# Performance work log

Measured on AMD Instinct MI355X. Metric: run time of the kernel, lower is better.

## Reference

```python
import jax, jax.numpy as jnp
import numpy as np

WIN = 20  # patch_project window_size
HID = 128


def _lstm_layer(x, w_ih, w_hh, b_ih, b_hh):
    """x: [B,T,D] -> (outputs [B,T,H], final h [B,H]). PyTorch gate order i,f,g,o."""
    B = x.shape[0]
    H = w_hh.shape[1]
    # precompute input contribution for all timesteps: [B,T,4H]
    x_pre = jnp.einsum('btd,gd->btg', x, w_ih) + b_ih + b_hh

    def step(carry, xp):
        h, c = carry
        gates = xp + h @ w_hh.T  # [B,4H]
        i, f, g, o = jnp.split(gates, 4, axis=-1)
        i = jax.nn.sigmoid(i)
        f = jax.nn.sigmoid(f)
        g = jnp.tanh(g)
        o = jax.nn.sigmoid(o)
        c = f * c + i * g
        h = o * jnp.tanh(c)
        return (h, c), h

    h0 = jnp.zeros((B, H), x.dtype)
    c0 = jnp.zeros((B, H), x.dtype)
    (h_f, _), ys = jax.lax.scan(step, (h0, c0), x_pre.transpose(1, 0, 2))
    return ys.transpose(1, 0, 2), h_f


def setup_inputs() -> dict:
    key = jax.random.key(0)
    ks = jax.random.split(key, 20)
    B, S, C = 64, 2048, 32
    D_in = WIN * C          # 640
    D_p = D_in // 2         # 320
    H = HID
    label_len = 48
    s = 0.02
    inp = {
        'inputs': jax.random.normal(ks[0], (B, S, C), jnp.float32),
        '_x': jnp.zeros((B, 4), jnp.float32),
        'y': jnp.zeros((B, label_len), jnp.float32),
        '_y': jnp.zeros((B, 4), jnp.float32),
        'proj_w': jax.random.normal(ks[1], (D_p, D_in), jnp.float32) * s,
        'proj_b': jax.random.normal(ks[2], (D_p,), jnp.float32) * s,
        'w_ih0': jax.random.normal(ks[3], (4 * H, D_p), jnp.float32) * s,
        'w_hh0': jax.random.normal(ks[4], (4 * H, H), jnp.float32) * s,
        'b_ih0': jax.random.normal(ks[5], (4 * H,), jnp.float32) * s,
        'b_hh0': jax.random.normal(ks[6], (4 * H,), jnp.float32) * s,
        'w_ih_rest': jax.random.normal(ks[7], (3, 4 * H, H), jnp.float32) * s,
        'w_hh_rest': jax.random.normal(ks[8], (3, 4 * H, H), jnp.float32) * s,
        'b_ih_rest': jax.random.normal(ks[9], (3, 4 * H), jnp.float32) * s,
        'b_hh_rest': jax.random.normal(ks[10], (3, 4 * H), jnp.float32) * s,
        'out_w': jax.random.normal(ks[11], (label_len, H), jnp.float32) * s,
        'out_b': jax.random.normal(ks[12], (label_len,), jnp.float32) * s,
    }
    return inp


def reference(inputs, _x, y, _y, proj_w, proj_b, w_ih0, w_hh0, b_ih0, b_hh0,
              w_ih_rest, w_hh_rest, b_ih_rest, b_hh_rest, out_w, out_b):
    B, S, C = inputs.shape
    L_out = S - WIN
    idx = jnp.arange(L_out)[:, None] + jnp.arange(WIN)[None, :]
    windows = inputs[:, idx, :].reshape(B, L_out, WIN * C)
    # projection1 (dropout is inference no-op)
    x = jnp.einsum('btd,pd->btp', windows, proj_w) + proj_b
    # 4-layer LSTM (dropout between layers is inference no-op)
    x, h = _lstm_layer(x, w_ih0, w_hh0, b_ih0, b_hh0)
    for l in range(3):
        x, h = _lstm_layer(x, w_ih_rest[l], w_hh_rest[l], b_ih_rest[l], b_hh_rest[l])
    # final hidden state of last layer -> [B,1,H] -> output layer -> [B,1,label_len]
    out = h[:, None, :] @ out_w.T + out_b
    return out
```

## Files before the change

### kernel.cpp

```cpp
#include <hip/hip_runtime.h>
#include <stdint.h>
#include <stddef.h>

typedef __bf16 bf16_t;
typedef bf16_t bf16x8 __attribute__((ext_vector_type(8)));
typedef bf16_t bf16x4 __attribute__((ext_vector_type(4)));
typedef float  f32x4  __attribute__((ext_vector_type(4)));

#define T_STEPS 2028
#define SEQ     2048
#define CIN     32
#define NG      32
#define MB      2
#define CH      32
#define NCH     64
#define RING    4

#define OFF_EFFW   0u
#define OFF_BIAS   655360u
#define OFF_WHH    663552u
#define OFF_WIH    1187840u
#define OFF_HFIN   1581056u
#define OFF_CNT    1613824u
#define OFF_XRING  1638400u
#define OFF_YRING  35192832u

__device__ __forceinline__ int endk(int k) {
  int e = (k + 1) * CH;
  return e > T_STEPS ? T_STEPS : e;
}

__device__ __forceinline__ void spin_ge(uint32_t* p, uint32_t tgt) {
  while (atomicAdd(p, 0u) < tgt) __builtin_amdgcn_s_sleep(2);
}
__device__ __forceinline__ void publish(uint32_t* p, uint32_t v) {
  __builtin_amdgcn_fence(__ATOMIC_RELEASE, "agent");
  atomicMax(p, v);
}

__device__ __forceinline__ float fsigm(float x) {
  return __builtin_amdgcn_rcpf(1.0f + __builtin_amdgcn_exp2f(x * -1.44269504089f));
}
__device__ __forceinline__ float ftanh(float x) {
  return 1.0f - 2.0f * __builtin_amdgcn_rcpf(1.0f + __builtin_amdgcn_exp2f(x * 2.88539008178f));
}

__device__ __forceinline__ bf16x8 ldg8(const bf16_t* p) { return *(const bf16x8*)p; }
__device__ __forceinline__ bf16x4 ldg4(const bf16_t* p) { return *(const bf16x4*)p; }

__device__ __forceinline__ bf16x8 ldg_cvt8(const float* p) {
  const f32x4 a = *(const f32x4*)p;
  const f32x4 b = *(const f32x4*)(p + 4);
  bf16x8 r;
  r[0] = (bf16_t)a[0]; r[1] = (bf16_t)a[1]; r[2] = (bf16_t)a[2]; r[3] = (bf16_t)a[3];
  r[4] = (bf16_t)b[0]; r[5] = (bf16_t)b[1]; r[6] = (bf16_t)b[2]; r[7] = (bf16_t)b[3];
  return r;
}


__global__ void k_prep_misc(const float* __restrict__ w_hh0,
                            const float* __restrict__ w_ih_rest,
                            const float* __restrict__ w_hh_rest,
                            const float* __restrict__ b_ih_rest,
                            const float* __restrict__ b_hh_rest,
                            uint8_t* __restrict__ ws) {
  const int bid = blockIdx.x;
  const int l = bid >> 9;
  const int p = bid & 511;
  const int orig = (p & 3) * 128 + (p >> 2);
  const int tid = threadIdx.x;
  bf16_t* whh = (bf16_t*)(ws + OFF_WHH);
  bf16_t* wih = (bf16_t*)(ws + OFF_WIH);
  float* bias = (float*)(ws + OFF_BIAS);
  const float* src = (l == 0) ? (w_hh0 + orig * 128)
                              : (w_hh_rest + ((size_t)(l - 1) * 512 + orig) * 128);
  whh[((size_t)l * 512 + p) * 128 + tid] = (bf16_t)src[tid];
  if (l < 3)
    wih[((size_t)l * 512 + p) * 128 + tid] = (bf16_t)w_ih_rest[((size_t)l * 512 + orig) * 128 + tid];
  if (l >= 1 && tid == 0)
    bias[l * 512 + p] = b_ih_rest[(l - 1) * 512 + orig] + b_hh_rest[(l - 1) * 512 + orig];
  if (bid == 0) {
    uint32_t* cnt = (uint32_t*)(ws + OFF_CNT);
    for (int i = tid; i < 12 * 32 * 16; i += 128) cnt[i] = 0;
  }
}

__global__ void k_prep_effw(const float* __restrict__ proj_w,
                            const float* __restrict__ proj_b,
                            const float* __restrict__ w_ih0,
                            const float* __restrict__ b_ih0,
                            const float* __restrict__ b_hh0,
                            uint8_t* __restrict__ ws) {
  __shared__ float wr[320];
  const int p = blockIdx.x;
  const int orig = (p & 3) * 128 + (p >> 2);
  const int tid = threadIdx.x;
  for (int i = tid; i < 320; i += 256) wr[i] = w_ih0[(size_t)orig * 320 + i];
  __syncthreads();
  bf16_t* effw = (bf16_t*)(ws + OFF_EFFW);
  for (int kk = tid; kk < 640; kk += 256) {
    float a = 0.f;
    for (int z = 0; z < 320; ++z) a += wr[z] * proj_w[(size_t)z * 640 + kk];
    effw[(size_t)p * 640 + kk] = (bf16_t)a;
  }
  if (tid == 0) {
    float a = 0.f;
    for (int z = 0; z < 320; ++z) a += wr[z] * proj_b[z];
    ((float*)(ws + OFF_BIAS))[p] = a + b_ih0[orig] + b_hh0[orig];
  }
}

__global__ __launch_bounds__(256, 1) void k_pipeline(const float* __restrict__ in,
                                                     uint8_t* __restrict__ ws) {
  __shared__ __align__(16) bf16_t h_lds[2][16][136];
  __shared__ f32x4 gate_buf[4][2][32];

  const int s = blockIdx.x >> 5;
  const int g = blockIdx.x & 31;
  const int tid = threadIdx.x;
  const int lane = tid & 63;
  const int w = tid >> 6;
  const int q = lane >> 4;
  const int ln = lane & 15;

  uint32_t* cnt = (uint32_t*)(ws + OFF_CNT);
  bf16_t* xring = (bf16_t*)(ws + OFF_XRING);
  bf16_t* yring = (bf16_t*)(ws + OFF_YRING);

  if (s == 0) {
    const bf16_t* effw = (const bf16_t*)(ws + OFF_EFFW);
    uint32_t* my = cnt + (0 * NG + g) * 16;
    uint32_t* guard = cnt + (1 * NG + g) * 16;
    for (int k = 0; k < NCH; ++k) {
      if (tid == 0 && k >= RING) spin_ge(guard, (uint32_t)endk(k - RING));
      __syncthreads();
      const int t0 = k * CH;
      f32x4 acc[4][8];
#pragma unroll
      for (int mt = 0; mt < 4; ++mt)
#pragma unroll
        for (int nt = 0; nt < 8; ++nt) acc[mt][nt] = (f32x4){0.f, 0.f, 0.f, 0.f};
#pragma unroll
      for (int kt = 0; kt < 20; ++kt) {
        bf16x8 bfr[8];
#pragma unroll
        for (int nt = 0; nt < 8; ++nt)
          bfr[nt] = ldg8(effw + (size_t)((w * 8 + nt) * 16 + ln) * 640 + kt * 32 + q * 8);
#pragma unroll
        for (int mt = 0; mt < 4; ++mt) {
          int m = mt * 16 + ln;
          int trel = m >> 1, bb = m & 1;
          int tt = t0 + trel; if (tt > T_STEPS - 1) tt = T_STEPS - 1;
          bf16x8 afr = ldg_cvt8(in + (size_t)((g * MB + bb) * SEQ + tt + kt) * CIN + q * 8);
#pragma unroll
          for (int nt = 0; nt < 8; ++nt)
            acc[mt][nt] = __builtin_amdgcn_mfma_f32_16x16x32_bf16(afr, bfr[nt], acc[mt][nt], 0, 0, 0);
        }
      }
      bf16_t* xs = xring + (size_t)((0 * NG + g) * RING + (k & 3)) * (64 * 512);
#pragma unroll
      for (int mt = 0; mt < 4; ++mt)
#pragma unroll
        for (int nt = 0; nt < 8; ++nt)
#pragma unroll
          for (int r = 0; r < 4; ++r)
            xs[(size_t)(mt * 16 + q * 4 + r) * 512 + (w * 8 + nt) * 16 + ln] = (bf16_t)acc[mt][nt][r];
      __syncthreads();
      if (tid == 0) publish(my, (uint32_t)endk(k));
    }
  } else if (s <= 4) {
    const int l = s - 1;
    const bf16_t* whh = (const bf16_t*)(ws + OFF_WHH) + (size_t)l * 512 * 128;
    bf16x8 wfr[8][4];
#pragma unroll
    for (int mt = 0; mt < 8; ++mt)
#pragma unroll
      for (int kt = 0; kt < 4; ++kt)
        wfr[mt][kt] = ldg8(whh + (size_t)(w * 128 + mt * 16 + ln) * 128 + kt * 32 + q * 8);
    const int b_ep = lane >> 5;
    const int j_loc = lane & 31;
    const int jg = w * 32 + j_loc;
    f32x4 biasq = *(const f32x4*)((const float*)(ws + OFF_BIAS) + l * 512 + 4 * jg);
    float c = 0.f;
    {
      bf16_t* hz = &h_lds[0][0][0];
      for (int i = tid; i < 2 * 16 * 136; i += 256) hz[i] = (bf16_t)0.f;
    }
    __syncthreads();
    uint32_t* my = cnt + ((1 + l) * NG + g) * 16;
    uint32_t* prod = (l == 0) ? (cnt + (0 * NG + g) * 16) : (cnt + ((4 + l) * NG + g) * 16);
    uint32_t* yguard = cnt + ((5 + l) * NG + g) * 16;
    float* hfin = (float*)(ws + OFF_HFIN);
    const int ly = (l < 3) ? l : 0;

    for (int k = 0; k < NCH; ++k) {
      const int t0 = k * CH;
      const int tlen = (T_STEPS - t0 < CH) ? (T_STEPS - t0) : CH;
      if (tid == 0) {
        spin_ge(prod, (uint32_t)(t0 + tlen));
        if (l < 3 && k >= RING) spin_ge(yguard, (uint32_t)endk(k - RING));
        __builtin_amdgcn_fence(__ATOMIC_ACQUIRE, "agent");
      }
      __syncthreads();
      const bf16_t* xlane = xring + (size_t)((l * NG + g) * RING + (k & 3)) * (64 * 512)
                            + b_ep * 512 + 4 * jg;
      bf16_t* ylane = yring + (size_t)((ly * NG + g) * RING + (k & 3)) * (64 * 128)
                      + b_ep * 128 + jg;

      if (tlen == CH) {
        for (int half = 0; half < 2; ++half) {
          const int tb = t0 + half * 16;
          bf16x4 xq[16];
#pragma unroll
          for (int t = 0; t < 16; ++t) xq[t] = ldg4(xlane + (size_t)(half * 16 + t) * 1024);
          bf16_t yv[16];
#pragma unroll
          for (int t = 0; t < 16; ++t) {
            const int buf = (tb + t) & 1;
            f32x4 acc[8];
#pragma unroll
            for (int mt = 0; mt < 8; ++mt) acc[mt] = (f32x4){0.f, 0.f, 0.f, 0.f};
#pragma unroll
            for (int kt = 0; kt < 3; ++kt) {
              bf16x8 hk = *(const bf16x8*)&h_lds[buf][ln][kt * 32 + q * 8];
#pragma unroll
              for (int mt = 0; mt < 8; ++mt)
                acc[mt] = __builtin_amdgcn_mfma_f32_16x16x32_bf16(wfr[mt][kt], hk, acc[mt], 0, 0, 0);
            }
            {
              bf16x8 hk3 = *(const bf16x8*)&h_lds[buf][ln][3 * 32 + q * 8];
#pragma unroll
              for (int mt = 0; mt < 8; ++mt) {
                acc[mt] = __builtin_amdgcn_mfma_f32_16x16x32_bf16(wfr[mt][3], hk3, acc[mt], 0, 0, 0);
                if (ln < MB) gate_buf[w][ln][mt * 4 + q] = acc[mt];
              }
            }
            f32x4 gq = gate_buf[w][b_ep][j_loc];
            float gi = fsigm(gq[0] + (float)xq[t][0] + biasq[0]);
            float gf = fsigm(gq[1] + (float)xq[t][1] + biasq[1]);
            float gg = ftanh(gq[2] + (float)xq[t][2] + biasq[2]);
            float go = fsigm(gq[3] + (float)xq[t][3] + biasq[3]);
            c = gf * c + gi * gg;
            float hv = go * ftanh(c);
            h_lds[buf ^ 1][b_ep][jg] = (bf16_t)hv;
            yv[t] = (bf16_t)hv;
            asm volatile("s_waitcnt lgkmcnt(0)\n\ts_barrier" ::: "memory");
          }
          if (l < 3) {
#pragma unroll
            for (int t = 0; t < 16; ++t)
              ylane[(size_t)(half * 16 + t) * 256] = yv[t];
          }
        }
      } else {
        for (int trel = 0; trel < tlen; ++trel) {
          const int t = t0 + trel;
          const int buf = t & 1;
          bf16x4 xqs = ldg4(xlane + (size_t)trel * 1024);
          f32x4 acc[8];
#pragma unroll
          for (int mt = 0; mt < 8; ++mt) acc[mt] = (f32x4){0.f, 0.f, 0.f, 0.f};
#pragma unroll
          for (int kt = 0; kt < 4; ++kt) {
            bf16x8 hk = *(const bf16x8*)&h_lds[buf][ln][kt * 32 + q * 8];
#pragma unroll
            for (int mt = 0; mt < 8; ++mt)
              acc[mt] = __builtin_amdgcn_mfma_f32_16x16x32_bf16(wfr[mt][kt], hk, acc[mt], 0, 0, 0);
          }
          if (ln < MB) {
#pragma unroll
            for (int mt = 0; mt < 8; ++mt)
              gate_buf[w][ln][mt * 4 + q] = acc[mt];
          }
          f32x4 gq = gate_buf[w][b_ep][j_loc];
          float gi = fsigm(gq[0] + (float)xqs[0] + biasq[0]);
          float gf = fsigm(gq[1] + (float)xqs[1] + biasq[1]);
          float gg = ftanh(gq[2] + (float)xqs[2] + biasq[2]);
          float go = fsigm(gq[3] + (float)xqs[3] + biasq[3]);
          c = gf * c + gi * gg;
          float hv = go * ftanh(c);
          h_lds[buf ^ 1][b_ep][jg] = (bf16_t)hv;
          if (l < 3) ylane[(size_t)trel * 256] = (bf16_t)hv;
          if (l == 3 && t == T_STEPS - 1) hfin[(g * MB + b_ep) * 128 + jg] = hv;
          asm volatile("s_waitcnt lgkmcnt(0)\n\ts_barrier" ::: "memory");
        }
      }
      __syncthreads();
      if (tid == 0) publish(my, (uint32_t)(t0 + tlen));
    }
  } else {
    const int l = s - 4;
    const bf16_t* wih = (const bf16_t*)(ws + OFF_WIH) + (size_t)(l - 1) * 512 * 128;
    bf16x8 bfr[8][4];
#pragma unroll
    for (int nt = 0; nt < 8; ++nt)
#pragma unroll
      for (int kt = 0; kt < 4; ++kt)
        bfr[nt][kt] = ldg8(wih + (size_t)((w * 8 + nt) * 16 + ln) * 128 + kt * 32 + q * 8);
    uint32_t* my = cnt + ((4 + l) * NG + g) * 16;
    uint32_t* prod = cnt + (l * NG + g) * 16;
    uint32_t* xguard = cnt + ((1 + l) * NG + g) * 16;
    for (int k = 0; k < NCH; ++k) {
      if (tid == 0) {
        spin_ge(prod, (uint32_t)endk(k));
        if (k >= RING) spin_ge(xguard, (uint32_t)endk(k - RING));
        __builtin_amdgcn_fence(__ATOMIC_ACQUIRE, "agent");
      }
      __syncthreads();
      const bf16_t* ys = yring + (size_t)(((l - 1) * NG + g) * RING + (k & 3)) * (64 * 128);
      bf16_t* xs = xring + (size_t)((l * NG + g) * RING + (k & 3)) * (64 * 512);
      bf16x8 afr[4][4];
#pragma unroll
      for (int mt = 0; mt < 4; ++mt)
#pragma unroll
        for (int kt = 0; kt < 4; ++kt)
          afr[mt][kt] = ldg8(ys + (size_t)(mt * 16 + ln) * 128 + kt * 32 + q * 8);
#pragma unroll
      for (int mt = 0; mt < 4; ++mt) {
        f32x4 a8[8];
#pragma unroll
        for (int nt = 0; nt < 8; ++nt) a8[nt] = (f32x4){0.f, 0.f, 0.f, 0.f};
#pragma unroll
        for (int kt = 0; kt < 4; ++kt) {
#pragma unroll
          for (int nt = 0; nt < 8; ++nt)
            a8[nt] = __builtin_amdgcn_mfma_f32_16x16x32_bf16(afr[mt][kt], bfr[nt][kt], a8[nt], 0, 0, 0);
        }
#pragma unroll
        for (int nt = 0; nt < 8; ++nt)
#pragma unroll
          for (int r = 0; r < 4; ++r)
            xs[(size_t)(mt * 16 + q * 4 + r) * 512 + (w * 8 + nt) * 16 + ln] = (bf16_t)a8[nt][r];
      }
      __syncthreads();
      if (tid == 0) publish(my, (uint32_t)endk(k));
    }
  }
}

__global__ void k_out(const float* __restrict__ out_w,
                      const float* __restrict__ out_b,
                      const uint8_t* __restrict__ ws,
                      float* __restrict__ out) {
  const int idx = blockIdx.x * 256 + threadIdx.x;
  const int b = idx / 48, o = idx % 48;
  const float* h = (const float*)(ws + OFF_HFIN) + b * 128;
  const float* wrow = out_w + (size_t)o * 128;
  float a = out_b[o];
  for (int j = 0; j < 128; ++j) a += h[j] * wrow[j];
  out[idx] = a;
}

extern "C" void kernel_launch(void* const* d_in, const int* in_sizes, int n_in,
                              void* d_out, int out_size, void* d_ws, size_t ws_size,
                              hipStream_t stream) {
  (void)in_sizes; (void)n_in; (void)out_size; (void)ws_size;
  const float* inputs    = (const float*)d_in[0];
  const float* proj_w    = (const float*)d_in[4];
  const float* proj_b    = (const float*)d_in[5];
  const float* w_ih0     = (const float*)d_in[6];
  const float* w_hh0     = (const float*)d_in[7];
  const float* b_ih0     = (const float*)d_in[8];
  const float* b_hh0     = (const float*)d_in[9];
  const float* w_ih_rest = (const float*)d_in[10];
  const float* w_hh_rest = (const float*)d_in[11];
  const float* b_ih_rest = (const float*)d_in[12];
  const float* b_hh_rest = (const float*)d_in[13];
  const float* out_w     = (const float*)d_in[14];
  const float* out_b     = (const float*)d_in[15];
  uint8_t* ws = (uint8_t*)d_ws;
  float* out = (float*)d_out;

  k_prep_misc<<<dim3(2048), dim3(128), 0, stream>>>(w_hh0, w_ih_rest, w_hh_rest,
                                                    b_ih_rest, b_hh_rest, ws);
  k_prep_effw<<<dim3(512), dim3(256), 0, stream>>>(proj_w, proj_b, w_ih0, b_ih0, b_hh0, ws);
  k_pipeline<<<dim3(256), dim3(256), 0, stream>>>(inputs, ws);
  k_out<<<dim3(12), dim3(256), 0, stream>>>(out_w, out_b, ws, out);
}
```

Before: 2.762 ms.

## Halve pipeline chunk size and fuse output layer into recurrent kernel

Cuts the time-chunk size shared by the projection, recurrence and input-GEMM stages from 32 to 16 steps and shrinks the ring buffers and GEMM tiles to match. Smaller chunks let each LSTM layer start sooner after the layer before it, which shortens the pipeline fill and drain across the four stacked layers. The final output projection now runs inside the last recurrent layer's block from shared memory, which removes the separate kernel launch and the global round trip for the final hidden state. The cost is twice as many inter-block synchronisation handshakes and smaller, less efficient GEMM chunks.

```diff
diff --git a/kernel.cpp b/kernel.cpp
--- a/kernel.cpp
+++ b/kernel.cpp
@@ -12,15 +12,14 @@
 #define CIN     32
 #define NG      32
 #define MB      2
-#define CH      32
-#define NCH     64
+#define CH      16
+#define NCH     127
 #define RING    4
 
 #define OFF_EFFW   0u
 #define OFF_BIAS   655360u
 #define OFF_WHH    663552u
 #define OFF_WIH    1187840u
-#define OFF_HFIN   1581056u
 #define OFF_CNT    1613824u
 #define OFF_XRING  1638400u
 #define OFF_YRING  35192832u
@@ -111,9 +110,13 @@
 }
 
 __global__ __launch_bounds__(256, 1) void k_pipeline(const float* __restrict__ in,
+                                                     const float* __restrict__ out_w,
+                                                     const float* __restrict__ out_b,
+                                                     float* __restrict__ out,
                                                      uint8_t* __restrict__ ws) {
   __shared__ __align__(16) bf16_t h_lds[2][16][136];
   __shared__ f32x4 gate_buf[4][2][32];
+  __shared__ float hfl[2][128];
 
   const int s = blockIdx.x >> 5;
   const int g = blockIdx.x & 31;
@@ -135,9 +138,9 @@
       if (tid == 0 && k >= RING) spin_ge(guard, (uint32_t)endk(k - RING));
       __syncthreads();
       const int t0 = k * CH;
-      f32x4 acc[4][8];
-#pragma unroll
-      for (int mt = 0; mt < 4; ++mt)
+      f32x4 acc[2][8];
+#pragma unroll
+      for (int mt = 0; mt < 2; ++mt)
 #pragma unroll
         for (int nt = 0; nt < 8; ++nt) acc[mt][nt] = (f32x4){0.f, 0.f, 0.f, 0.f};
 #pragma unroll
@@ -147,7 +150,7 @@
         for (int nt = 0; nt < 8; ++nt)
           bfr[nt] = ldg8(effw + (size_t)((w * 8 + nt) * 16 + ln) * 640 + kt * 32 + q * 8);
 #pragma unroll
-        for (int mt = 0; mt < 4; ++mt) {
+        for (int mt = 0; mt < 2; ++mt) {
           int m = mt * 16 + ln;
           int trel = m >> 1, bb = m & 1;
           int tt = t0 + trel; if (tt > T_STEPS - 1) tt = T_STEPS - 1;
@@ -157,9 +160,9 @@
             acc[mt][nt] = __builtin_amdgcn_mfma_f32_16x16x32_bf16(afr, bfr[nt], acc[mt][nt], 0, 0, 0);
         }
       }
-      bf16_t* xs = xring + (size_t)((0 * NG + g) * RING + (k & 3)) * (64 * 512);
-#pragma unroll
-      for (int mt = 0; mt < 4; ++mt)
+      bf16_t* xs = xring + (size_t)((0 * NG + g) * RING + (k & 3)) * (32 * 512);
+#pragma unroll
+      for (int mt = 0; mt < 2; ++mt)
 #pragma unroll
         for (int nt = 0; nt < 8; ++nt)
 #pragma unroll
@@ -190,7 +193,6 @@
     uint32_t* my = cnt + ((1 + l) * NG + g) * 16;
     uint32_t* prod = (l == 0) ? (cnt + (0 * NG + g) * 16) : (cnt + ((4 + l) * NG + g) * 16);
     uint32_t* yguard = cnt + ((5 + l) * NG + g) * 16;
-    float* hfin = (float*)(ws + OFF_HFIN);
     const int ly = (l < 3) ? l : 0;
 
     for (int k = 0; k < NCH; ++k) {
@@ -202,55 +204,52 @@
         __builtin_amdgcn_fence(__ATOMIC_ACQUIRE, "agent");
       }
       __syncthreads();
-      const bf16_t* xlane = xring + (size_t)((l * NG + g) * RING + (k & 3)) * (64 * 512)
+      const bf16_t* xlane = xring + (size_t)((l * NG + g) * RING + (k & 3)) * (32 * 512)
                             + b_ep * 512 + 4 * jg;
-      bf16_t* ylane = yring + (size_t)((ly * NG + g) * RING + (k & 3)) * (64 * 128)
+      bf16_t* ylane = yring + (size_t)((ly * NG + g) * RING + (k & 3)) * (32 * 128)
                       + b_ep * 128 + jg;
 
       if (tlen == CH) {
-        for (int half = 0; half < 2; ++half) {
-          const int tb = t0 + half * 16;
-          bf16x4 xq[16];
-#pragma unroll
-          for (int t = 0; t < 16; ++t) xq[t] = ldg4(xlane + (size_t)(half * 16 + t) * 1024);
-          bf16_t yv[16];
-#pragma unroll
-          for (int t = 0; t < 16; ++t) {
-            const int buf = (tb + t) & 1;
-            f32x4 acc[8];
-#pragma unroll
-            for (int mt = 0; mt < 8; ++mt) acc[mt] = (f32x4){0.f, 0.f, 0.f, 0.f};
-#pragma unroll
-            for (int kt = 0; kt < 3; ++kt) {
-              bf16x8 hk = *(const bf16x8*)&h_lds[buf][ln][kt * 32 + q * 8];
-#pragma unroll
-              for (int mt = 0; mt < 8; ++mt)
-                acc[mt] = __builtin_amdgcn_mfma_f32_16x16x32_bf16(wfr[mt][kt], hk, acc[mt], 0, 0, 0);
+        bf16x4 xq[16];
+#pragma unroll
+        for (int t = 0; t < 16; ++t) xq[t] = ldg4(xlane + (size_t)t * 1024);
+        bf16_t yv[16];
+#pragma unroll
+        for (int t = 0; t < 16; ++t) {
+          const int buf = (t0 + t) & 1;
+          f32x4 acc[8];
+#pragma unroll
+          for (int mt = 0; mt < 8; ++mt) acc[mt] = (f32x4){0.f, 0.f, 0.f, 0.f};
+#pragma unroll
+          for (int kt = 0; kt < 3; ++kt) {
+            bf16x8 hk = *(const bf16x8*)&h_lds[buf][ln][kt * 32 + q * 8];
+#pragma unroll
+            for (int mt = 0; mt < 8; ++mt)
+              acc[mt] = __builtin_amdgcn_mfma_f32_16x16x32_bf16(wfr[mt][kt], hk, acc[mt], 0, 0, 0);
+          }
+          {
+            bf16x8 hk3 = *(const bf16x8*)&h_lds[buf][ln][3 * 32 + q * 8];
+#pragma unroll
+            for (int mt = 0; mt < 8; ++mt) {
+              acc[mt] = __builtin_amdgcn_mfma_f32_16x16x32_bf16(wfr[mt][3], hk3, acc[mt], 0, 0, 0);
+              if (ln < MB) gate_buf[w][ln][mt * 4 + q] = acc[mt];
             }
-            {
-              bf16x8 hk3 = *(const bf16x8*)&h_lds[buf][ln][3 * 32 + q * 8];
-#pragma unroll
-              for (int mt = 0; mt < 8; ++mt) {
-                acc[mt] = __builtin_amdgcn_mfma_f32_16x16x32_bf16(wfr[mt][3], hk3, acc[mt], 0, 0, 0);
-                if (ln < MB) gate_buf[w][ln][mt * 4 + q] = acc[mt];
-              }
-            }
-            f32x4 gq = gate_buf[w][b_ep][j_loc];
-            float gi = fsigm(gq[0] + (float)xq[t][0] + biasq[0]);
-            float gf = fsigm(gq[1] + (float)xq[t][1] + biasq[1]);
-            float gg = ftanh(gq[2] + (float)xq[t][2] + biasq[2]);
-            float go = fsigm(gq[3] + (float)xq[t][3] + biasq[3]);
-            c = gf * c + gi * gg;
-            float hv = go * ftanh(c);
-            h_lds[buf ^ 1][b_ep][jg] = (bf16_t)hv;
-            yv[t] = (bf16_t)hv;
-            asm volatile("s_waitcnt lgkmcnt(0)\n\ts_barrier" ::: "memory");
           }
-          if (l < 3) {
-#pragma unroll
-            for (int t = 0; t < 16; ++t)
-              ylane[(size_t)(half * 16 + t) * 256] = yv[t];
-          }
+          f32x4 gq = gate_buf[w][b_ep][j_loc];
+          float gi = fsigm(gq[0] + (float)xq[t][0] + biasq[0]);
+          float gf = fsigm(gq[1] + (float)xq[t][1] + biasq[1]);
+          float gg = ftanh(gq[2] + (float)xq[t][2] + biasq[2]);
+          float go = fsigm(gq[3] + (float)xq[t][3] + biasq[3]);
+          c = gf * c + gi * gg;
+          float hv = go * ftanh(c);
+          h_lds[buf ^ 1][b_ep][jg] = (bf16_t)hv;
+          yv[t] = (bf16_t)hv;
+          asm volatile("s_waitcnt lgkmcnt(0)\n\ts_barrier" ::: "memory");
+        }
+        if (l < 3) {
+#pragma unroll
+          for (int t = 0; t < 16; ++t)
+            ylane[(size_t)t * 256] = yv[t];
         }
       } else {
         for (int trel = 0; trel < tlen; ++trel) {
@@ -281,12 +280,24 @@
           float hv = go * ftanh(c);
           h_lds[buf ^ 1][b_ep][jg] = (bf16_t)hv;
           if (l < 3) ylane[(size_t)trel * 256] = (bf16_t)hv;
-          if (l == 3 && t == T_STEPS - 1) hfin[(g * MB + b_ep) * 128 + jg] = hv;
+          if (l == 3 && t == T_STEPS - 1) hfl[b_ep][jg] = hv;
           asm volatile("s_waitcnt lgkmcnt(0)\n\ts_barrier" ::: "memory");
         }
       }
       __syncthreads();
       if (tid == 0) publish(my, (uint32_t)(t0 + tlen));
+    }
+
+    if (l == 3) {
+      __syncthreads();
+      if (tid < 96) {
+        const int b_loc = tid / 48, o = tid % 48;
+        const float* wrow = out_w + (size_t)o * 128;
+        float a = out_b[o];
+#pragma unroll 4
+        for (int j = 0; j < 128; ++j) a += hfl[b_loc][j] * wrow[j];
+        out[(size_t)(g * MB + b_loc) * 48 + o] = a;
+      }
     }
   } else {
     const int l = s - 4;
@@ -307,16 +318,16 @@
         __builtin_amdgcn_fence(__ATOMIC_ACQUIRE, "agent");
       }
       __syncthreads();
-      const bf16_t* ys = yring + (size_t)(((l - 1) * NG + g) * RING + (k & 3)) * (64 * 128);
-      bf16_t* xs = xring + (size_t)((l * NG + g) * RING + (k & 3)) * (64 * 512);
-      bf16x8 afr[4][4];
-#pragma unroll
-      for (int mt = 0; mt < 4; ++mt)
+      const bf16_t* ys = yring + (size_t)(((l - 1) * NG + g) * RING + (k & 3)) * (32 * 128);
+      bf16_t* xs = xring + (size_t)((l * NG + g) * RING + (k & 3)) * (32 * 512);
+      bf16x8 afr[2][4];
+#pragma unroll
+      for (int mt = 0; mt < 2; ++mt)
 #pragma unroll
         for (int kt = 0; kt < 4; ++kt)
           afr[mt][kt] = ldg8(ys + (size_t)(mt * 16 + ln) * 128 + kt * 32 + q * 8);
 #pragma unroll
-      for (int mt = 0; mt < 4; ++mt) {
+      for (int mt = 0; mt < 2; ++mt) {
         f32x4 a8[8];
 #pragma unroll
         for (int nt = 0; nt < 8; ++nt) a8[nt] = (f32x4){0.f, 0.f, 0.f, 0.f};
@@ -336,19 +347,6 @@
       if (tid == 0) publish(my, (uint32_t)endk(k));
     }
   }
-}
-
-__global__ void k_out(const float* __restrict__ out_w,
-                      const float* __restrict__ out_b,
-                      const uint8_t* __restrict__ ws,
-                      float* __restrict__ out) {
-  const int idx = blockIdx.x * 256 + threadIdx.x;
-  const int b = idx / 48, o = idx % 48;
-  const float* h = (const float*)(ws + OFF_HFIN) + b * 128;
-  const float* wrow = out_w + (size_t)o * 128;
-  float a = out_b[o];
-  for (int j = 0; j < 128; ++j) a += h[j] * wrow[j];
-  out[idx] = a;
 }
 
 extern "C" void kernel_launch(void* const* d_in, const int* in_sizes, int n_in,
@@ -374,6 +372,5 @@
   k_prep_misc<<<dim3(2048), dim3(128), 0, stream>>>(w_hh0, w_ih_rest, w_hh_rest,
                                                     b_ih_rest, b_hh_rest, ws);
   k_prep_effw<<<dim3(512), dim3(256), 0, stream>>>(proj_w, proj_b, w_ih0, b_ih0, b_hh0, ws);
-  k_pipeline<<<dim3(256), dim3(256), 0, stream>>>(inputs, ws);
-  k_out<<<dim3(12), dim3(256), 0, stream>>>(out_w, out_b, ws, out);
-}
+  k_pipeline<<<dim3(256), dim3(256), 0, stream>>>(inputs, out_w, out_b, out, ws);
+}
```

Result: slower. 4.000 ms (+44.8%).
